# Optimization experiments

Measured on AMD Instinct MI355X. Metric: run time of the kernel, lower is better.

Reference implementation:

```python
import jax, jax.numpy as jnp
import numpy as np

T, B, E, H, C, N, V, O = 256, 512, 256, 256, 256, 128, 256, 256
EPS = 1e-8  # torch F.cosine_similarity eps


def setup_inputs() -> dict:
    key = jax.random.key(0)
    ks = jax.random.split(key, 7)
    s = 0.05
    return {
        "x": jax.random.normal(ks[0], (T, B, E), jnp.float32),
        "W1": jax.random.normal(ks[1], (E + V, H), jnp.float32) * s,
        "b1": jnp.zeros((H,), jnp.float32),
        "W2": jax.random.normal(ks[2], (H, C), jnp.float32) * s,
        "b2": jnp.zeros((C,), jnp.float32),
        "Wr": jax.random.normal(ks[3], (C, V), jnp.float32) * s,
        "br": jnp.zeros((V,), jnp.float32),
        "Ww": jax.random.normal(ks[4], (C, 2 * V), jnp.float32) * s,
        "bw": jnp.zeros((2 * V,), jnp.float32),
        "Wo": jax.random.normal(ks[5], (C + V, O), jnp.float32) * s,
        "bo": jnp.zeros((O,), jnp.float32),
        "init_read": jnp.zeros((B, V), jnp.float32),
        "mem0": jnp.zeros((B, N, V), jnp.float32),
    }


def _address(k, mem):
    # cosine similarity of key k [B,V] against each memory row [B,N,V], then softmax (NTM 3.3)
    dot = jnp.einsum('bv,bnv->bn', k, mem)
    kn = jnp.maximum(jnp.linalg.norm(k, axis=-1, keepdims=True), EPS)   # [B,1]
    mn = jnp.maximum(jnp.linalg.norm(mem, axis=-1), EPS)                # [B,N]
    return jax.nn.softmax(dot / (kn * mn), axis=-1)


def reference(x, W1, b1, W2, b2, Wr, br, Ww, bw, Wo, bo, init_read, mem0):
    def step(carry, xt):
        mem, read = carry  # mem [B,N,V], read [B,V]; xt [B,E]
        ci = jnp.concatenate([xt, read], axis=-1)            # controller input [B,E+V]
        h = jax.nn.relu(ci @ W1 + b1)
        co = h @ W2 + b2                                     # controller output [B,C]
        # read head (uses pre-write memory)
        k = co @ Wr + br
        w = _address(k, mem)
        r = jnp.einsum('bn,bnv->bv', w, mem)
        # write head: split into write key and value
        o = co @ Ww + bw
        kw, v = o[:, :V], o[:, V:]
        ww = _address(kw, mem)
        mem = mem + ww[:, :, None] * v[:, None, :]           # rank-1 per-batch write
        out = jnp.concatenate([co, r], axis=-1) @ Wo + bo    # [B,O]
        return (mem, r), out

    (_, _), outs = jax.lax.scan(step, (mem0, init_read), x)
    return outs  # [T,B,O]
```

## Files before the change

### kernel.cpp

```cpp
#include <hip/hip_runtime.h>
#include <stdint.h>

typedef unsigned short u16;
typedef unsigned int   u32;

#define T_STEPS 256
#define B_TOT   512
#define EDIM    256
#define NSLOT   128
#define VDIM    256
#define ODIM    256

#define OFF_W1 0
#define OFF_W2 65536
#define OFF_WR 98304
#define OFF_WW 131072
#define OFF_WO 196608
#define W_TOTAL_U32 262144

#define SLOTU32 132
#define SLOTQ   33
#define MEMROWU32 (NSLOT * SLOTU32)
#define MEMROWQ   (NSLOT * SLOTQ)
#define DLDS (2 * MEMROWU32 * 4)

__device__ __forceinline__ float bflo(u32 u) { return __uint_as_float(u << 16); }
__device__ __forceinline__ float bfhi(u32 u) { return __uint_as_float(u & 0xffff0000u); }
__device__ __forceinline__ u32 f2bfbits(float f) {
    u32 a = __float_as_uint(f);
    return (a + 0x7fffu + ((a >> 16) & 1u)) >> 16;
}
__device__ __forceinline__ u32 pkbf(float lo, float hi) {
    u32 a = __float_as_uint(lo), b = __float_as_uint(hi);
    a = a + 0x7fffu + ((a >> 16) & 1u);
    b = b + 0x7fffu + ((b >> 16) & 1u);
    return (a >> 16) | (b & 0xffff0000u);
}
__device__ __forceinline__ u32 cvtpk(float lo, float hi) {
    u32 r;
    asm("v_cvt_pk_bf16_f32 %0, %1, %2" : "=v"(r) : "v"(lo), "v"(hi));
    return r;
}
__device__ __forceinline__ float dot2bf(u32 a, u32 b, float c) {
    float d;
    asm("v_dot2_f32_bf16 %0, %1, %2, %3" : "=v"(d) : "v"(a), "v"(b), "v"(c));
    return d;
}

__global__ void cvt_weights(const float* __restrict__ W1, const float* __restrict__ W2,
                            const float* __restrict__ Wr, const float* __restrict__ Ww,
                            const float* __restrict__ Wo, u32* __restrict__ dst) {
    int idx = blockIdx.x * 256 + threadIdx.x;
    const float* src; int local, shape, C;
    if      (idx < 65536)  { src = W1; local = idx;          shape = 0; C = 256; }
    else if (idx < 98304)  { src = W2; local = idx - 65536;  shape = 1; C = 256; }
    else if (idx < 131072) { src = Wr; local = idx - 98304;  shape = 1; C = 256; }
    else if (idx < 196608) { src = Ww; local = idx - 131072; shape = 2; C = 512; }
    else                   { src = Wo; local = idx - 196608; shape = 0; C = 256; }
    const int q4 = local >> 2, e = local & 3;
    const int tid = q4 & 1023, blk = q4 >> 10;
    int kp, c;
    if (shape == 1) {
        const int j = blk;
        const int jg = tid >> 2, s = tid & 3;
        kp = s * 32 + ((j + s) & 7) * 4 + e;
        c  = jg;
    } else {
        const int j = blk >> 1, half = blk & 1;
        int jg, s;
        if (shape == 0) { jg = tid >> 3; s = tid & 7; }
        else            { jg = tid >> 2; s = tid & 3; }
        kp = s * 32 + ((j + s) & 7) * 4 + half * 2 + (e >> 1);
        c  = jg * 2 + (e & 1);
    }
    dst[idx] = pkbf(src[(2 * kp) * C + c], src[(2 * kp + 1) * C + c]);
}

template<int DST, bool RELU>
__device__ __forceinline__ void mvA(const uint4* __restrict__ W,
                                    const u16* __restrict__ src,
                                    const float* __restrict__ bias,
                                    u16* dst,
                                    float* g0, float* g1) {
    const int tid = threadIdx.x;
    const int jg = tid >> 3, s = tid & 7;
    const uint4* a0 = reinterpret_cast<const uint4*>(src) + s * 8;
    const uint4* a1 = a0 + 64;
    float a00 = 0.f, a01 = 0.f, a10 = 0.f, a11 = 0.f;
#pragma unroll 2
    for (int j = 0; j < 8; ++j) {
        const int aj = (j + s) & 7;
        uint4 w0 = W[(2 * j    ) * 1024 + tid];
        uint4 w1 = W[(2 * j + 1) * 1024 + tid];
        uint4 x0 = a0[aj];
        uint4 x1 = a1[aj];
        a00 = dot2bf(x0.x, w0.x, a00); a01 = dot2bf(x0.x, w0.y, a01);
        a00 = dot2bf(x0.y, w0.z, a00); a01 = dot2bf(x0.y, w0.w, a01);
        a00 = dot2bf(x0.z, w1.x, a00); a01 = dot2bf(x0.z, w1.y, a01);
        a00 = dot2bf(x0.w, w1.z, a00); a01 = dot2bf(x0.w, w1.w, a01);
        a10 = dot2bf(x1.x, w0.x, a10); a11 = dot2bf(x1.x, w0.y, a11);
        a10 = dot2bf(x1.y, w0.z, a10); a11 = dot2bf(x1.y, w0.w, a11);
        a10 = dot2bf(x1.z, w1.x, a10); a11 = dot2bf(x1.z, w1.y, a11);
        a10 = dot2bf(x1.w, w1.z, a10); a11 = dot2bf(x1.w, w1.w, a11);
    }
    a00 += __shfl_xor(a00, 1); a00 += __shfl_xor(a00, 2); a00 += __shfl_xor(a00, 4);
    a01 += __shfl_xor(a01, 1); a01 += __shfl_xor(a01, 2); a01 += __shfl_xor(a01, 4);
    a10 += __shfl_xor(a10, 1); a10 += __shfl_xor(a10, 2); a10 += __shfl_xor(a10, 4);
    a11 += __shfl_xor(a11, 1); a11 += __shfl_xor(a11, 2); a11 += __shfl_xor(a11, 4);
    if (s == 0) {
        const float bb0 = bias[2 * jg], bb1 = bias[2 * jg + 1];
        float v00 = a00 + bb0, v01 = a01 + bb1;
        float v10 = a10 + bb0, v11 = a11 + bb1;
        if (RELU) {
            v00 = fmaxf(v00, 0.f); v01 = fmaxf(v01, 0.f);
            v10 = fmaxf(v10, 0.f); v11 = fmaxf(v11, 0.f);
        }
        if constexpr (DST == 1) {
            reinterpret_cast<u32*>(dst)[jg]       = cvtpk(v00, v01);
            reinterpret_cast<u32*>(dst)[128 + jg] = cvtpk(v10, v11);
        } else {
            reinterpret_cast<float2*>(g0)[jg] = make_float2(v00, v01);
            reinterpret_cast<float2*>(g1)[jg] = make_float2(v10, v11);
        }
    }
    if constexpr (DST != 2) __syncthreads();
}

template<int AS4, bool BAR>
__device__ __forceinline__ void mvB(const uint4* __restrict__ W,
                                    const u16* __restrict__ src,
                                    const float* __restrict__ bias,
                                    u16* dst, int dstride) {
    const int tid = threadIdx.x;
    const int jg = tid >> 2, s = tid & 3;
    const uint4* a0 = reinterpret_cast<const uint4*>(src) + s * 8;
    const uint4* a1 = a0 + AS4;
    float r0 = 0.f, r1 = 0.f;
#pragma unroll 4
    for (int j = 0; j < 8; ++j) {
        const int aj = (j + s) & 7;
        uint4 w  = W[j * 1024 + tid];
        uint4 x0 = a0[aj];
        uint4 x1 = a1[aj];
        r0 = dot2bf(x0.x, w.x, r0); r0 = dot2bf(x0.y, w.y, r0);
        r0 = dot2bf(x0.z, w.z, r0); r0 = dot2bf(x0.w, w.w, r0);
        r1 = dot2bf(x1.x, w.x, r1); r1 = dot2bf(x1.y, w.y, r1);
        r1 = dot2bf(x1.z, w.z, r1); r1 = dot2bf(x1.w, w.w, r1);
    }
    r0 += __shfl_xor(r0, 1); r0 += __shfl_xor(r0, 2);
    r1 += __shfl_xor(r1, 1); r1 += __shfl_xor(r1, 2);
    if (s == 0) {
        const float bb = bias[jg];
        dst[jg]           = (u16)f2bfbits(r0 + bb);
        dst[dstride + jg] = (u16)f2bfbits(r1 + bb);
    }
    if constexpr (BAR) __syncthreads();
}

__device__ __forceinline__ void mvC(const uint4* __restrict__ W,
                                    const u16* __restrict__ src,
                                    const float* __restrict__ bias,
                                    u16* dst) {
    const int tid = threadIdx.x;
    const int jg = tid >> 2, s = tid & 3;
    const uint4* a0 = reinterpret_cast<const uint4*>(src) + s * 8;
    const uint4* a1 = a0 + 64;
    float a00 = 0.f, a01 = 0.f, a10 = 0.f, a11 = 0.f;
#pragma unroll 2
    for (int j = 0; j < 8; ++j) {
        const int aj = (j + s) & 7;
        uint4 w0 = W[(2 * j    ) * 1024 + tid];
        uint4 w1 = W[(2 * j + 1) * 1024 + tid];
        uint4 x0 = a0[aj];
        uint4 x1 = a1[aj];
        a00 = dot2bf(x0.x, w0.x, a00); a01 = dot2bf(x0.x, w0.y, a01);
        a00 = dot2bf(x0.y, w0.z, a00); a01 = dot2bf(x0.y, w0.w, a01);
        a00 = dot2bf(x0.z, w1.x, a00); a01 = dot2bf(x0.z, w1.y, a01);
        a00 = dot2bf(x0.w, w1.z, a00); a01 = dot2bf(x0.w, w1.w, a01);
        a10 = dot2bf(x1.x, w0.x, a10); a11 = dot2bf(x1.x, w0.y, a11);
        a10 = dot2bf(x1.y, w0.z, a10); a11 = dot2bf(x1.y, w0.w, a11);
        a10 = dot2bf(x1.z, w1.x, a10); a11 = dot2bf(x1.z, w1.y, a11);
        a10 = dot2bf(x1.w, w1.z, a10); a11 = dot2bf(x1.w, w1.w, a11);
    }
    a00 += __shfl_xor(a00, 1); a00 += __shfl_xor(a00, 2);
    a01 += __shfl_xor(a01, 1); a01 += __shfl_xor(a01, 2);
    a10 += __shfl_xor(a10, 1); a10 += __shfl_xor(a10, 2);
    a11 += __shfl_xor(a11, 1); a11 += __shfl_xor(a11, 2);
    if (s == 0) {
        u32* d32 = reinterpret_cast<u32*>(dst);
        d32[jg]       = cvtpk(a00 + bias[2 * jg], a01 + bias[2 * jg + 1]);
        d32[256 + jg] = cvtpk(a10 + bias[2 * jg], a11 + bias[2 * jg + 1]);
    }
    __syncthreads();
}

__global__ __launch_bounds__(1024, 4)
void ntm_main(const float* __restrict__ x, const u32* __restrict__ Wb,
              const float* __restrict__ b1, const float* __restrict__ b2,
              const float* __restrict__ br, const float* __restrict__ bw,
              const float* __restrict__ bo,
              const float* __restrict__ init_read, const float* __restrict__ mem0,
              float* __restrict__ out) {
    extern __shared__ u16 s_mem[];
    __shared__ __align__(16) u16 s_cib[2 * 512];
    __shared__ __align__(16) u16 s_hb [2 * 256];
    __shared__ __align__(16) u16 s_crb[2 * 512];
    __shared__ __align__(16) u16 s_kvb[2 * 256];
    __shared__ __align__(16) u16 s_ovb[2 * 512];
    __shared__ __align__(16) float s_dotr[2 * 128], s_dotw[2 * 128], s_mn2[2 * 128];
    __shared__ __align__(16) float s_wr[2 * 128], s_ww[2 * 128];

    const int tid = threadIdx.x;
    const int b   = blockIdx.x;
    u32*   m32  = reinterpret_cast<u32*>(s_mem);
    uint4* memq = reinterpret_cast<uint4*>(s_mem);

    const uint4* W1q = reinterpret_cast<const uint4*>(Wb + OFF_W1);
    const uint4* W2q = reinterpret_cast<const uint4*>(Wb + OFF_W2);
    const uint4* Wrq = reinterpret_cast<const uint4*>(Wb + OFF_WR);
    const uint4* Wwq = reinterpret_cast<const uint4*>(Wb + OFF_WW);
    const uint4* Woq = reinterpret_cast<const uint4*>(Wb + OFF_WO);

#pragma unroll 1
    for (int it = 0; it < 32; ++it) {
        int li  = it * 1024 + tid;
        int row = li >> 14, rem = li & 16383;
        int n = rem >> 7, c = rem & 127;
        float2 g = reinterpret_cast<const float2*>(mem0 + ((size_t)(2 * b + row) << 15))[rem];
        m32[row * MEMROWU32 + n * SLOTU32 + c] = pkbf(g.x, g.y);
    }
    if (tid < 256) {
        int row = tid >> 7, i = tid & 127;
        float2 g = reinterpret_cast<const float2*>(init_read + ((size_t)(2 * b + row) << 8))[i];
        reinterpret_cast<u32*>(s_cib)[row * 256 + 128 + i] = pkbf(g.x, g.y);
    }
    float2 gx = make_float2(0.f, 0.f);
    if (tid < 256) {
        int row = tid >> 7, i = tid & 127;
        gx = reinterpret_cast<const float2*>(x + (size_t)(2 * b + row) * EDIM)[i];
    }
    __syncthreads();

#pragma unroll 1
    for (int t = 0; t < T_STEPS; ++t) {
        if (tid < 256) {
            int row = tid >> 7, i = tid & 127;
            reinterpret_cast<u32*>(s_cib)[row * 256 + i] = cvtpk(gx.x, gx.y);
        }
        __syncthreads();

        mvA<1, true>(W1q, s_cib, b1, s_hb, nullptr, nullptr);

        if (t + 1 < T_STEPS && tid < 256) {
            int row = tid >> 7, i = tid & 127;
            gx = reinterpret_cast<const float2*>(
                x + (size_t)(t + 1) * (B_TOT * EDIM) + (size_t)(2 * b + row) * EDIM)[i];
        }

        mvB<32, true >(W2q, s_hb,  b2, s_crb, 512);
        mvB<64, false>(Wrq, s_crb, br, s_kvb, 256);
        mvC(Wwq, s_crb, bw, s_ovb);

        {
            const int row = tid >> 9, n = (tid >> 2) & 127, vq = tid & 3;
            const uint4* mq  = memq + row * MEMROWQ + n * SLOTQ;
            const uint4* kq  = reinterpret_cast<const uint4*>(s_kvb) + row * 32;
            const uint4* kwq = reinterpret_cast<const uint4*>(s_ovb) + row * 64;
            float dr = 0.f, dw = 0.f, s2 = 0.f;
#pragma unroll
            for (int ih = 0; ih < 4; ++ih) {
                const int e = vq * 2 + ih * 8;
                uint4 m0 = mq[e], m1 = mq[e + 1];
                uint4 ka = kq[e], kb = kq[e + 1];
                uint4 wa = kwq[e], wb = kwq[e + 1];
                dr = dot2bf(m0.x, ka.x, dr); dr = dot2bf(m0.y, ka.y, dr);
                dr = dot2bf(m0.z, ka.z, dr); dr = dot2bf(m0.w, ka.w, dr);
                dr = dot2bf(m1.x, kb.x, dr); dr = dot2bf(m1.y, kb.y, dr);
                dr = dot2bf(m1.z, kb.z, dr); dr = dot2bf(m1.w, kb.w, dr);
                dw = dot2bf(m0.x, wa.x, dw); dw = dot2bf(m0.y, wa.y, dw);
                dw = dot2bf(m0.z, wa.z, dw); dw = dot2bf(m0.w, wa.w, dw);
                dw = dot2bf(m1.x, wb.x, dw); dw = dot2bf(m1.y, wb.y, dw);
                dw = dot2bf(m1.z, wb.z, dw); dw = dot2bf(m1.w, wb.w, dw);
                s2 = dot2bf(m0.x, m0.x, s2); s2 = dot2bf(m0.y, m0.y, s2);
                s2 = dot2bf(m0.z, m0.z, s2); s2 = dot2bf(m0.w, m0.w, s2);
                s2 = dot2bf(m1.x, m1.x, s2); s2 = dot2bf(m1.y, m1.y, s2);
                s2 = dot2bf(m1.z, m1.z, s2); s2 = dot2bf(m1.w, m1.w, s2);
            }
            dr += __shfl_xor(dr, 1); dr += __shfl_xor(dr, 2);
            dw += __shfl_xor(dw, 1); dw += __shfl_xor(dw, 2);
            s2 += __shfl_xor(s2, 1); s2 += __shfl_xor(s2, 2);
            if (vq == 0) {
                s_dotr[row * 128 + n] = dr;
                s_dotw[row * 128 + n] = dw;
                s_mn2 [row * 128 + n] = s2;
            }
        }
        __syncthreads();

        if (tid < 256) {
            const int row = tid >> 7, key = (tid >> 6) & 1, lane = tid & 63;
            const uint2* kv2 = key ? (reinterpret_cast<const uint2*>(s_ovb) + row * 128)
                                   : (reinterpret_cast<const uint2*>(s_kvb) + row * 64);
            uint2 kk = kv2[lane];
            float q = dot2bf(kk.x, kk.x, 0.f);
            q = dot2bf(kk.y, kk.y, q);
#pragma unroll
            for (int m = 1; m < 64; m <<= 1) q += __shfl_xor(q, m);
            float kn = fmaxf(sqrtf(q), 1e-8f);
            const float* dot = (key ? s_dotw : s_dotr) + row * 128;
            const float* mn2 = s_mn2 + row * 128;
            int n0 = lane, n1 = lane + 64;
            float mn0 = fmaxf(sqrtf(mn2[n0]), 1e-8f);
            float mn1 = fmaxf(sqrtf(mn2[n1]), 1e-8f);
            float av0 = dot[n0] / (kn * mn0);
            float av1 = dot[n1] / (kn * mn1);
            float mx = fmaxf(av0, av1);
#pragma unroll
            for (int m = 1; m < 64; m <<= 1) mx = fmaxf(mx, __shfl_xor(mx, m));
            float e0 = __expf(av0 - mx), e1 = __expf(av1 - mx);
            float sm = e0 + e1;
#pragma unroll
            for (int m = 1; m < 64; m <<= 1) sm += __shfl_xor(sm, m);
            float inv = 1.0f / sm;
            float* wdst = (key ? s_ww : s_wr) + row * 128;
            wdst[n0] = e0 * inv;
            wdst[n1] = e1 * inv;
        }
        __syncthreads();

        {
            const int row = tid >> 9, vc = (tid >> 2) & 127, ns = tid & 3;
            const u32* mrow = m32 + row * MEMROWU32;
            const float* wp = s_wr + row * 128;
            float r0 = 0.f, r1 = 0.f;
#pragma unroll 4
            for (int j = 0; j < 32; ++j) {
                const int slot = ns + 4 * j;
                u32 m = mrow[slot * SLOTU32 + vc];
                float wj = wp[slot];
                r0 = fmaf(bflo(m), wj, r0);
                r1 = fmaf(bfhi(m), wj, r1);
            }
            r0 += __shfl_xor(r0, 1); r0 += __shfl_xor(r0, 2);
            r1 += __shfl_xor(r1, 1); r1 += __shfl_xor(r1, 2);
            if (ns == 0) {
                u32 p = cvtpk(r0, r1);
                reinterpret_cast<u32*>(s_cib)[row * 256 + 128 + vc] = p;
                reinterpret_cast<u32*>(s_crb)[row * 256 + 128 + vc] = p;
            }
        }
        __syncthreads();

        {
            const int row = tid >> 9, n = (tid >> 2) & 127, vq = tid & 3;
            uint4* mq = memq + row * MEMROWQ + n * SLOTQ;
            const uint4* vv = reinterpret_cast<const uint4*>(s_ovb) + row * 64 + 32;
            const float wwn = s_ww[row * 128 + n];
#pragma unroll
            for (int ih = 0; ih < 4; ++ih) {
                const int e = vq * 2 + ih * 8;
                uint4 m0 = mq[e], m1 = mq[e + 1];
                uint4 v0 = vv[e], v1 = vv[e + 1];
                u32* pm0 = reinterpret_cast<u32*>(&m0);
                const u32* pv0 = reinterpret_cast<const u32*>(&v0);
#pragma unroll
                for (int q = 0; q < 4; ++q) {
                    float o0 = fmaf(bflo(pv0[q]), wwn, bflo(pm0[q]));
                    float o1 = fmaf(bfhi(pv0[q]), wwn, bfhi(pm0[q]));
                    pm0[q] = cvtpk(o0, o1);
                }
                u32* pm1 = reinterpret_cast<u32*>(&m1);
                const u32* pv1 = reinterpret_cast<const u32*>(&v1);
#pragma unroll
                for (int q = 0; q < 4; ++q) {
                    float o0 = fmaf(bflo(pv1[q]), wwn, bflo(pm1[q]));
                    float o1 = fmaf(bfhi(pv1[q]), wwn, bfhi(pm1[q]));
                    pm1[q] = cvtpk(o0, o1);
                }
                mq[e] = m0; mq[e + 1] = m1;
            }
        }
        __syncthreads();

        mvA<2, false>(Woq, s_crb, bo, nullptr,
                      out + (size_t)t * (B_TOT * ODIM) + (size_t)(2 * b) * ODIM,
                      out + (size_t)t * (B_TOT * ODIM) + (size_t)(2 * b + 1) * ODIM);
    }
}

extern "C" void kernel_launch(void* const* d_in, const int* in_sizes, int n_in,
                              void* d_out, int out_size, void* d_ws, size_t ws_size,
                              hipStream_t stream) {
    (void)in_sizes; (void)n_in; (void)out_size; (void)ws_size;
    const float* x         = (const float*)d_in[0];
    const float* W1        = (const float*)d_in[1];
    const float* b1        = (const float*)d_in[2];
    const float* W2        = (const float*)d_in[3];
    const float* b2        = (const float*)d_in[4];
    const float* Wr        = (const float*)d_in[5];
    const float* br        = (const float*)d_in[6];
    const float* Ww        = (const float*)d_in[7];
    const float* bw        = (const float*)d_in[8];
    const float* Wo        = (const float*)d_in[9];
    const float* bo        = (const float*)d_in[10];
    const float* init_read = (const float*)d_in[11];
    const float* mem0      = (const float*)d_in[12];
    float* out = (float*)d_out;
    u32* wb = (u32*)d_ws;

    hipLaunchKernelGGL(cvt_weights, dim3(W_TOTAL_U32 / 256), dim3(256), 0, stream,
                       W1, W2, Wr, Ww, Wo, wb);

    (void)hipFuncSetAttribute(reinterpret_cast<const void*>(ntm_main),
                              hipFuncAttributeMaxDynamicSharedMemorySize, DLDS);

    hipLaunchKernelGGL(ntm_main, dim3(B_TOT / 2), dim3(1024), DLDS, stream,
                       x, wb, b1, b2, br, bw, bo, init_read, mem0, out);
}
```

Before: 4.256 ms.

## Restructure matvecs to 4 columns per lane with DPP reductions and preloaded weights

Reorganizes the per-step bf16 matrix-vector products so each thread group computes four output columns over a 16-way (or 8-way) K split. All weight vectors for a thread are loaded into registers up front, and the weight pre-conversion layout is remapped to match. Cross-lane shuffle reductions are replaced with DPP adds, and outputs are written as packed or float4 stores. The x staging into shared memory now overlaps with the softmax phase, which removes one barrier per step. In exchange, register pressure rises sharply (16 uint4 of weights per thread), which may lower occupancy or cause spills.

New measurement: 11.66 ms. 174% more time.

```diff
diff --git a/kernel.cpp b/kernel.cpp
--- a/kernel.cpp
+++ b/kernel.cpp
@@ -47,31 +47,53 @@
     return d;
 }
 
+template<int CTRL>
+__device__ __forceinline__ float dppadd(float v) {
+    int t = __builtin_amdgcn_update_dpp(0, __float_as_int(v), CTRL, 0xf, 0xf, true);
+    return v + __int_as_float(t);
+}
+__device__ __forceinline__ float red16(float v) {
+    v = dppadd<0xB1>(v);
+    v = dppadd<0x4E>(v);
+    v = dppadd<0x141>(v);
+    v = dppadd<0x140>(v);
+    return v;
+}
+__device__ __forceinline__ float red8(float v) {
+    v = dppadd<0xB1>(v); v = dppadd<0x4E>(v); v = dppadd<0x141>(v);
+    return v;
+}
+__device__ __forceinline__ float red4(float v) {
+    v = dppadd<0xB1>(v); v = dppadd<0x4E>(v);
+    return v;
+}
+
 __global__ void cvt_weights(const float* __restrict__ W1, const float* __restrict__ W2,
                             const float* __restrict__ Wr, const float* __restrict__ Ww,
                             const float* __restrict__ Wo, u32* __restrict__ dst) {
     int idx = blockIdx.x * 256 + threadIdx.x;
-    const float* src; int local, shape, C;
-    if      (idx < 65536)  { src = W1; local = idx;          shape = 0; C = 256; }
-    else if (idx < 98304)  { src = W2; local = idx - 65536;  shape = 1; C = 256; }
-    else if (idx < 131072) { src = Wr; local = idx - 98304;  shape = 1; C = 256; }
-    else if (idx < 196608) { src = Ww; local = idx - 131072; shape = 2; C = 512; }
-    else                   { src = Wo; local = idx - 196608; shape = 0; C = 256; }
-    const int q4 = local >> 2, e = local & 3;
+    const float* src; int local, shape;
+    if      (idx < 65536)  { src = W1; local = idx;          shape = 0; }
+    else if (idx < 98304)  { src = W2; local = idx - 65536;  shape = 1; }
+    else if (idx < 131072) { src = Wr; local = idx - 98304;  shape = 1; }
+    else if (idx < 196608) { src = Ww; local = idx - 131072; shape = 2; }
+    else                   { src = Wo; local = idx - 196608; shape = 0; }
+    const int e = local & 3, q4 = local >> 2;
     const int tid = q4 & 1023, blk = q4 >> 10;
-    int kp, c;
-    if (shape == 1) {
-        const int j = blk;
-        const int jg = tid >> 2, s = tid & 3;
-        kp = s * 32 + ((j + s) & 7) * 4 + e;
-        c  = jg;
+    const int j = blk >> 2, ci = blk & 3;
+    int kp, c, C;
+    if (shape == 0) {
+        const int cq = tid >> 4, s = tid & 15;
+        kp = s * 16 + ((j + s) & 3) * 4 + e;
+        c  = cq * 4 + ci; C = 256;
+    } else if (shape == 1) {
+        const int cq = tid >> 4, s = tid & 15;
+        kp = s * 8 + ((j + s) & 1) * 4 + e;
+        c  = cq * 4 + ci; C = 256;
     } else {
-        const int j = blk >> 1, half = blk & 1;
-        int jg, s;
-        if (shape == 0) { jg = tid >> 3; s = tid & 7; }
-        else            { jg = tid >> 2; s = tid & 3; }
-        kp = s * 32 + ((j + s) & 7) * 4 + half * 2 + (e >> 1);
-        c  = jg * 2 + (e & 1);
+        const int cq = tid >> 3, s = tid & 7;
+        kp = s * 16 + ((j + s) & 3) * 4 + e;
+        c  = cq * 4 + ci; C = 512;
     }
     dst[idx] = pkbf(src[(2 * kp) * C + c], src[(2 * kp + 1) * C + c]);
 }
@@ -80,79 +102,94 @@
 __device__ __forceinline__ void mvA(const uint4* __restrict__ W,
                                     const u16* __restrict__ src,
                                     const float* __restrict__ bias,
-                                    u16* dst,
-                                    float* g0, float* g1) {
+                                    u32* __restrict__ dst,
+                                    float4* __restrict__ g0, float4* __restrict__ g1) {
     const int tid = threadIdx.x;
-    const int jg = tid >> 3, s = tid & 7;
-    const uint4* a0 = reinterpret_cast<const uint4*>(src) + s * 8;
+    const int cq = tid >> 4, s = tid & 15;
+    const uint4* a0 = reinterpret_cast<const uint4*>(src) + s * 4;
     const uint4* a1 = a0 + 64;
-    float a00 = 0.f, a01 = 0.f, a10 = 0.f, a11 = 0.f;
-#pragma unroll 2
-    for (int j = 0; j < 8; ++j) {
-        const int aj = (j + s) & 7;
-        uint4 w0 = W[(2 * j    ) * 1024 + tid];
-        uint4 w1 = W[(2 * j + 1) * 1024 + tid];
-        uint4 x0 = a0[aj];
-        uint4 x1 = a1[aj];
-        a00 = dot2bf(x0.x, w0.x, a00); a01 = dot2bf(x0.x, w0.y, a01);
-        a00 = dot2bf(x0.y, w0.z, a00); a01 = dot2bf(x0.y, w0.w, a01);
-        a00 = dot2bf(x0.z, w1.x, a00); a01 = dot2bf(x0.z, w1.y, a01);
-        a00 = dot2bf(x0.w, w1.z, a00); a01 = dot2bf(x0.w, w1.w, a01);
-        a10 = dot2bf(x1.x, w0.x, a10); a11 = dot2bf(x1.x, w0.y, a11);
-        a10 = dot2bf(x1.y, w0.z, a10); a11 = dot2bf(x1.y, w0.w, a11);
-        a10 = dot2bf(x1.z, w1.x, a10); a11 = dot2bf(x1.z, w1.y, a11);
-        a10 = dot2bf(x1.w, w1.z, a10); a11 = dot2bf(x1.w, w1.w, a11);
-    }
-    a00 += __shfl_xor(a00, 1); a00 += __shfl_xor(a00, 2); a00 += __shfl_xor(a00, 4);
-    a01 += __shfl_xor(a01, 1); a01 += __shfl_xor(a01, 2); a01 += __shfl_xor(a01, 4);
-    a10 += __shfl_xor(a10, 1); a10 += __shfl_xor(a10, 2); a10 += __shfl_xor(a10, 4);
-    a11 += __shfl_xor(a11, 1); a11 += __shfl_xor(a11, 2); a11 += __shfl_xor(a11, 4);
+    uint4 w[16];
+#pragma unroll
+    for (int u = 0; u < 16; ++u) w[u] = W[u * 1024 + tid];
+    float acc[8] = {0.f, 0.f, 0.f, 0.f, 0.f, 0.f, 0.f, 0.f};
+#pragma unroll
+    for (int j = 0; j < 4; ++j) {
+        const int rot = (j + s) & 3;
+        uint4 x0 = a0[rot], x1 = a1[rot];
+#pragma unroll
+        for (int ci = 0; ci < 4; ++ci) {
+            const uint4 ww = w[j * 4 + ci];
+            acc[ci * 2 + 0] = dot2bf(x0.x, ww.x, acc[ci * 2 + 0]);
+            acc[ci * 2 + 0] = dot2bf(x0.y, ww.y, acc[ci * 2 + 0]);
+            acc[ci * 2 + 0] = dot2bf(x0.z, ww.z, acc[ci * 2 + 0]);
+            acc[ci * 2 + 0] = dot2bf(x0.w, ww.w, acc[ci * 2 + 0]);
+            acc[ci * 2 + 1] = dot2bf(x1.x, ww.x, acc[ci * 2 + 1]);
+            acc[ci * 2 + 1] = dot2bf(x1.y, ww.y, acc[ci * 2 + 1]);
+            acc[ci * 2 + 1] = dot2bf(x1.z, ww.z, acc[ci * 2 + 1]);
+            acc[ci * 2 + 1] = dot2bf(x1.w, ww.w, acc[ci * 2 + 1]);
+        }
+    }
+#pragma unroll
+    for (int i = 0; i < 8; ++i) acc[i] = red16(acc[i]);
     if (s == 0) {
-        const float bb0 = bias[2 * jg], bb1 = bias[2 * jg + 1];
-        float v00 = a00 + bb0, v01 = a01 + bb1;
-        float v10 = a10 + bb0, v11 = a11 + bb1;
+        const float4 b4 = reinterpret_cast<const float4*>(bias)[cq];
+        float v00 = acc[0] + b4.x, v01 = acc[2] + b4.y, v02 = acc[4] + b4.z, v03 = acc[6] + b4.w;
+        float v10 = acc[1] + b4.x, v11 = acc[3] + b4.y, v12 = acc[5] + b4.z, v13 = acc[7] + b4.w;
         if (RELU) {
-            v00 = fmaxf(v00, 0.f); v01 = fmaxf(v01, 0.f);
-            v10 = fmaxf(v10, 0.f); v11 = fmaxf(v11, 0.f);
+            v00 = fmaxf(v00, 0.f); v01 = fmaxf(v01, 0.f); v02 = fmaxf(v02, 0.f); v03 = fmaxf(v03, 0.f);
+            v10 = fmaxf(v10, 0.f); v11 = fmaxf(v11, 0.f); v12 = fmaxf(v12, 0.f); v13 = fmaxf(v13, 0.f);
         }
         if constexpr (DST == 1) {
-            reinterpret_cast<u32*>(dst)[jg]       = cvtpk(v00, v01);
-            reinterpret_cast<u32*>(dst)[128 + jg] = cvtpk(v10, v11);
+            dst[cq * 2]           = cvtpk(v00, v01);
+            dst[cq * 2 + 1]       = cvtpk(v02, v03);
+            dst[128 + cq * 2]     = cvtpk(v10, v11);
+            dst[128 + cq * 2 + 1] = cvtpk(v12, v13);
         } else {
-            reinterpret_cast<float2*>(g0)[jg] = make_float2(v00, v01);
-            reinterpret_cast<float2*>(g1)[jg] = make_float2(v10, v11);
+            g0[cq] = make_float4(v00, v01, v02, v03);
+            g1[cq] = make_float4(v10, v11, v12, v13);
         }
     }
     if constexpr (DST != 2) __syncthreads();
 }
 
-template<int AS4, bool BAR>
+template<int AS4, int DS32, bool BAR>
 __device__ __forceinline__ void mvB(const uint4* __restrict__ W,
                                     const u16* __restrict__ src,
                                     const float* __restrict__ bias,
-                                    u16* dst, int dstride) {
+                                    u32* __restrict__ dst) {
     const int tid = threadIdx.x;
-    const int jg = tid >> 2, s = tid & 3;
-    const uint4* a0 = reinterpret_cast<const uint4*>(src) + s * 8;
+    const int cq = tid >> 4, s = tid & 15;
+    const uint4* a0 = reinterpret_cast<const uint4*>(src) + s * 2;
     const uint4* a1 = a0 + AS4;
-    float r0 = 0.f, r1 = 0.f;
-#pragma unroll 4
-    for (int j = 0; j < 8; ++j) {
-        const int aj = (j + s) & 7;
-        uint4 w  = W[j * 1024 + tid];
-        uint4 x0 = a0[aj];
-        uint4 x1 = a1[aj];
-        r0 = dot2bf(x0.x, w.x, r0); r0 = dot2bf(x0.y, w.y, r0);
-        r0 = dot2bf(x0.z, w.z, r0); r0 = dot2bf(x0.w, w.w, r0);
-        r1 = dot2bf(x1.x, w.x, r1); r1 = dot2bf(x1.y, w.y, r1);
-        r1 = dot2bf(x1.z, w.z, r1); r1 = dot2bf(x1.w, w.w, r1);
-    }
-    r0 += __shfl_xor(r0, 1); r0 += __shfl_xor(r0, 2);
-    r1 += __shfl_xor(r1, 1); r1 += __shfl_xor(r1, 2);
+    uint4 w[8];
+#pragma unroll
+    for (int u = 0; u < 8; ++u) w[u] = W[u * 1024 + tid];
+    float acc[8] = {0.f, 0.f, 0.f, 0.f, 0.f, 0.f, 0.f, 0.f};
+#pragma unroll
+    for (int j = 0; j < 2; ++j) {
+        const int rot = (j + s) & 1;
+        uint4 x0 = a0[rot], x1 = a1[rot];
+#pragma unroll
+        for (int ci = 0; ci < 4; ++ci) {
+            const uint4 ww = w[j * 4 + ci];
+            acc[ci * 2 + 0] = dot2bf(x0.x, ww.x, acc[ci * 2 + 0]);
+            acc[ci * 2 + 0] = dot2bf(x0.y, ww.y, acc[ci * 2 + 0]);
+            acc[ci * 2 + 0] = dot2bf(x0.z, ww.z, acc[ci * 2 + 0]);
+            acc[ci * 2 + 0] = dot2bf(x0.w, ww.w, acc[ci * 2 + 0]);
+            acc[ci * 2 + 1] = dot2bf(x1.x, ww.x, acc[ci * 2 + 1]);
+            acc[ci * 2 + 1] = dot2bf(x1.y, ww.y, acc[ci * 2 + 1]);
+            acc[ci * 2 + 1] = dot2bf(x1.z, ww.z, acc[ci * 2 + 1]);
+            acc[ci * 2 + 1] = dot2bf(x1.w, ww.w, acc[ci * 2 + 1]);
+        }
+    }
+#pragma unroll
+    for (int i = 0; i < 8; ++i) acc[i] = red16(acc[i]);
     if (s == 0) {
-        const float bb = bias[jg];
-        dst[jg]           = (u16)f2bfbits(r0 + bb);
-        dst[dstride + jg] = (u16)f2bfbits(r1 + bb);
+        const float4 b4 = reinterpret_cast<const float4*>(bias)[cq];
+        dst[cq * 2]            = cvtpk(acc[0] + b4.x, acc[2] + b4.y);
+        dst[cq * 2 + 1]        = cvtpk(acc[4] + b4.z, acc[6] + b4.w);
+        dst[DS32 + cq * 2]     = cvtpk(acc[1] + b4.x, acc[3] + b4.y);
+        dst[DS32 + cq * 2 + 1] = cvtpk(acc[5] + b4.z, acc[7] + b4.w);
     }
     if constexpr (BAR) __syncthreads();
 }
@@ -160,36 +197,40 @@
 __device__ __forceinline__ void mvC(const uint4* __restrict__ W,
                                     const u16* __restrict__ src,
                                     const float* __restrict__ bias,
-                                    u16* dst) {
+                                    u32* __restrict__ dst) {
     const int tid = threadIdx.x;
-    const int jg = tid >> 2, s = tid & 3;
-    const uint4* a0 = reinterpret_cast<const uint4*>(src) + s * 8;
+    const int cq = tid >> 3, s = tid & 7;
+    const uint4* a0 = reinterpret_cast<const uint4*>(src) + s * 4;
     const uint4* a1 = a0 + 64;
-    float a00 = 0.f, a01 = 0.f, a10 = 0.f, a11 = 0.f;
-#pragma unroll 2
-    for (int j = 0; j < 8; ++j) {
-        const int aj = (j + s) & 7;
-        uint4 w0 = W[(2 * j    ) * 1024 + tid];
-        uint4 w1 = W[(2 * j + 1) * 1024 + tid];
-        uint4 x0 = a0[aj];
-        uint4 x1 = a1[aj];
-        a00 = dot2bf(x0.x, w0.x, a00); a01 = dot2bf(x0.x, w0.y, a01);
-        a00 = dot2bf(x0.y, w0.z, a00); a01 = dot2bf(x0.y, w0.w, a01);
-        a00 = dot2bf(x0.z, w1.x, a00); a01 = dot2bf(x0.z, w1.y, a01);
-        a00 = dot2bf(x0.w, w1.z, a00); a01 = dot2bf(x0.w, w1.w, a01);
-        a10 = dot2bf(x1.x, w0.x, a10); a11 = dot2bf(x1.x, w0.y, a11);
-        a10 = dot2bf(x1.y, w0.z, a10); a11 = dot2bf(x1.y, w0.w, a11);
-        a10 = dot2bf(x1.z, w1.x, a10); a11 = dot2bf(x1.z, w1.y, a11);
-        a10 = dot2bf(x1.w, w1.z, a10); a11 = dot2bf(x1.w, w1.w, a11);
-    }
-    a00 += __shfl_xor(a00, 1); a00 += __shfl_xor(a00, 2);
-    a01 += __shfl_xor(a01, 1); a01 += __shfl_xor(a01, 2);
-    a10 += __shfl_xor(a10, 1); a10 += __shfl_xor(a10, 2);
-    a11 += __shfl_xor(a11, 1); a11 += __shfl_xor(a11, 2);
+    uint4 w[16];
+#pragma unroll
+    for (int u = 0; u < 16; ++u) w[u] = W[u * 1024 + tid];
+    float acc[8] = {0.f, 0.f, 0.f, 0.f, 0.f, 0.f, 0.f, 0.f};
+#pragma unroll
+    for (int j = 0; j < 4; ++j) {
+        const int rot = (j + s) & 3;
+        uint4 x0 = a0[rot], x1 = a1[rot];
+#pragma unroll
+        for (int ci = 0; ci < 4; ++ci) {
+            const uint4 ww = w[j * 4 + ci];
+            acc[ci * 2 + 0] = dot2bf(x0.x, ww.x, acc[ci * 2 + 0]);
+            acc[ci * 2 + 0] = dot2bf(x0.y, ww.y, acc[ci * 2 + 0]);
+            acc[ci * 2 + 0] = dot2bf(x0.z, ww.z, acc[ci * 2 + 0]);
+            acc[ci * 2 + 0] = dot2bf(x0.w, ww.w, acc[ci * 2 + 0]);
+            acc[ci * 2 + 1] = dot2bf(x1.x, ww.x, acc[ci * 2 + 1]);
+            acc[ci * 2 + 1] = dot2bf(x1.y, ww.y, acc[ci * 2 + 1]);
+            acc[ci * 2 + 1] = dot2bf(x1.z, ww.z, acc[ci * 2 + 1]);
+            acc[ci * 2 + 1] = dot2bf(x1.w, ww.w, acc[ci * 2 + 1]);
+        }
+    }
+#pragma unroll
+    for (int i = 0; i < 8; ++i) acc[i] = red8(acc[i]);
     if (s == 0) {
-        u32* d32 = reinterpret_cast<u32*>(dst);
-        d32[jg]       = cvtpk(a00 + bias[2 * jg], a01 + bias[2 * jg + 1]);
-        d32[256 + jg] = cvtpk(a10 + bias[2 * jg], a11 + bias[2 * jg + 1]);
+        const float4 b4 = reinterpret_cast<const float4*>(bias)[cq];
+        dst[cq * 2]           = cvtpk(acc[0] + b4.x, acc[2] + b4.y);
+        dst[cq * 2 + 1]       = cvtpk(acc[4] + b4.z, acc[6] + b4.w);
+        dst[256 + cq * 2]     = cvtpk(acc[1] + b4.x, acc[3] + b4.y);
+        dst[256 + cq * 2 + 1] = cvtpk(acc[5] + b4.z, acc[7] + b4.w);
     }
     __syncthreads();
 }
@@ -235,31 +276,26 @@
         reinterpret_cast<u32*>(s_cib)[row * 256 + 128 + i] = pkbf(g.x, g.y);
     }
     float2 gx = make_float2(0.f, 0.f);
-    if (tid < 256) {
-        int row = tid >> 7, i = tid & 127;
-        gx = reinterpret_cast<const float2*>(x + (size_t)(2 * b + row) * EDIM)[i];
+    if (tid >= 256 && tid < 512) {
+        const int local = tid - 256, row = local >> 7, i = local & 127;
+        gx = reinterpret_cast<const float2*>(x + ((size_t)(2 * b + row)) * EDIM)[i];
+        reinterpret_cast<u32*>(s_cib)[row * 256 + i] = pkbf(gx.x, gx.y);
     }
     __syncthreads();
 
 #pragma unroll 1
     for (int t = 0; t < T_STEPS; ++t) {
-        if (tid < 256) {
-            int row = tid >> 7, i = tid & 127;
-            reinterpret_cast<u32*>(s_cib)[row * 256 + i] = cvtpk(gx.x, gx.y);
-        }
-        __syncthreads();
-
-        mvA<1, true>(W1q, s_cib, b1, s_hb, nullptr, nullptr);
-
-        if (t + 1 < T_STEPS && tid < 256) {
-            int row = tid >> 7, i = tid & 127;
+        mvA<1, true>(W1q, s_cib, b1, reinterpret_cast<u32*>(s_hb), nullptr, nullptr);
+
+        if (t + 1 < T_STEPS && tid >= 256 && tid < 512) {
+            const int local = tid - 256, row = local >> 7, i = local & 127;
             gx = reinterpret_cast<const float2*>(
                 x + (size_t)(t + 1) * (B_TOT * EDIM) + (size_t)(2 * b + row) * EDIM)[i];
         }
 
-        mvB<32, true >(W2q, s_hb,  b2, s_crb, 512);
-        mvB<64, false>(Wrq, s_crb, br, s_kvb, 256);
-        mvC(Wwq, s_crb, bw, s_ovb);
+        mvB<32, 256, true >(W2q, s_hb,  b2, reinterpret_cast<u32*>(s_crb));
+        mvB<64, 128, false>(Wrq, s_crb, br, reinterpret_cast<u32*>(s_kvb));
+        mvC(Wwq, s_crb, bw, reinterpret_cast<u32*>(s_ovb));
 
         {
             const int row = tid >> 9, n = (tid >> 2) & 127, vq = tid & 3;
@@ -286,9 +322,7 @@
                 s2 = dot2bf(m1.x, m1.x, s2); s2 = dot2bf(m1.y, m1.y, s2);
                 s2 = dot2bf(m1.z, m1.z, s2); s2 = dot2bf(m1.w, m1.w, s2);
             }
-            dr += __shfl_xor(dr, 1); dr += __shfl_xor(dr, 2);
-            dw += __shfl_xor(dw, 1); dw += __shfl_xor(dw, 2);
-            s2 += __shfl_xor(s2, 1); s2 += __shfl_xor(s2, 2);
+            dr = red4(dr); dw = red4(dw); s2 = red4(s2);
             if (vq == 0) {
                 s_dotr[row * 128 + n] = dr;
                 s_dotw[row * 128 + n] = dw;
@@ -325,6 +359,9 @@
             float* wdst = (key ? s_ww : s_wr) + row * 128;
             wdst[n0] = e0 * inv;
             wdst[n1] = e1 * inv;
+        } else if (tid < 512) {
+            const int local = tid - 256, row = local >> 7, i = local & 127;
+            reinterpret_cast<u32*>(s_cib)[row * 256 + i] = cvtpk(gx.x, gx.y);
         }
         __syncthreads();
 
@@ -333,7 +370,7 @@
             const u32* mrow = m32 + row * MEMROWU32;
             const float* wp = s_wr + row * 128;
             float r0 = 0.f, r1 = 0.f;
-#pragma unroll 4
+#pragma unroll 8
             for (int j = 0; j < 32; ++j) {
                 const int slot = ns + 4 * j;
                 u32 m = mrow[slot * SLOTU32 + vc];
@@ -341,8 +378,7 @@
                 r0 = fmaf(bflo(m), wj, r0);
                 r1 = fmaf(bfhi(m), wj, r1);
             }
-            r0 += __shfl_xor(r0, 1); r0 += __shfl_xor(r0, 2);
-            r1 += __shfl_xor(r1, 1); r1 += __shfl_xor(r1, 2);
+            r0 = red4(r0); r1 = red4(r1);
             if (ns == 0) {
                 u32 p = cvtpk(r0, r1);
                 reinterpret_cast<u32*>(s_cib)[row * 256 + 128 + vc] = p;
@@ -383,8 +419,10 @@
         __syncthreads();
 
         mvA<2, false>(Woq, s_crb, bo, nullptr,
-                      out + (size_t)t * (B_TOT * ODIM) + (size_t)(2 * b) * ODIM,
-                      out + (size_t)t * (B_TOT * ODIM) + (size_t)(2 * b + 1) * ODIM);
+                      reinterpret_cast<float4*>(out + (size_t)t * (B_TOT * ODIM)
+                                                + (size_t)(2 * b) * ODIM),
+                      reinterpret_cast<float4*>(out + (size_t)t * (B_TOT * ODIM)
+                                                + (size_t)(2 * b + 1) * ODIM));
     }
 }
 
```
